# Kernel optimization log

Measured on AMD Instinct MI355X. Metric: run time of the kernel, lower is better.

## Reference

```python
import jax, jax.numpy as jnp
import numpy as np

HK, WK = 7, 11  # local_k


def _local_mask(H, W):
    # Equivalent to the torch buffer: 0 inside the hk x wk window centered on the
    # query position (for odd hk, wk), -inf outside. Shape (N, N), N = H*W.
    n = jnp.arange(H * W)
    hq, wq = n // W, n % W
    dh = jnp.abs(hq[:, None] - hq[None, :])
    dw = jnp.abs(wq[:, None] - wq[None, :])
    allowed = (dh <= HK // 2) & (dw <= WK // 2)
    return jnp.where(allowed, 0.0, -jnp.inf).astype(jnp.float32)


def setup_inputs() -> dict:
    key = jax.random.key(0)
    k1, k2, k3 = jax.random.split(key, 3)
    B, H, W, C = 8, 32, 64, 512
    N = H * W
    x = jax.random.normal(k1, (B, N, C), dtype=jnp.float32)
    qkv_w = jax.random.normal(k2, (3 * C, C), dtype=jnp.float32) * (C ** -0.5)
    proj_w = jax.random.normal(k3, (C, C), dtype=jnp.float32) * (C ** -0.5)
    proj_b = jnp.zeros((C,), dtype=jnp.float32)
    return {"x": x, "qkv_w": qkv_w, "proj_w": proj_w, "proj_b": proj_b, "H": H, "W": W}


def reference(x, qkv_w, proj_w, proj_b, H, W):
    B, N, C = x.shape
    num_heads = 8
    head_dim = C // num_heads
    scale = head_dim ** -0.5

    # qkv: Linear(dim, 3*dim, bias=False) -> (B, N, 3, heads, head_dim)
    qkv = (x @ qkv_w.T).reshape(B, N, 3, num_heads, head_dim)
    q = qkv[:, :, 0].transpose(0, 2, 1, 3) * scale  # (B, h, N, d)
    k = qkv[:, :, 1].transpose(0, 2, 1, 3)
    v = qkv[:, :, 2].transpose(0, 2, 1, 3)

    attn = jnp.einsum('bhnd,bhmd->bhnm', q, k)  # (B, h, N, N)
    attn = attn + _local_mask(H, W)  # broadcast over (B, h)
    attn = jax.nn.softmax(attn, axis=-1)

    out = jnp.einsum('bhnm,bhmd->bhnd', attn, v)  # (B, h, N, d)
    out = out.transpose(0, 2, 1, 3).reshape(B, N, C)
    return out @ proj_w.T + proj_b
```

## Files before the change

kernel.cpp:

```cpp
#include <hip/hip_runtime.h>
#include <hip/hip_bf16.h>

#define B_SZ 8
#define H_SZ 32
#define W_SZ 64
#define N_SZ 2048
#define C_SZ 512
#define NH 8
#define HD 64

using u16 = unsigned short;
typedef __attribute__((ext_vector_type(8))) short s16x8;
typedef __attribute__((ext_vector_type(4))) float f32x4;

__device__ __forceinline__ float bf2f(u16 u) {
    union { unsigned int i; float f; } c; c.i = ((unsigned int)u) << 16; return c.f;
}
__device__ __forceinline__ u16 f2bf(float f) {
    union { float f; unsigned int i; } c; c.f = f;
    unsigned int r = c.i + 0x7fffu + ((c.i >> 16) & 1u);
    return (u16)(r >> 16);
}

#define GLL16(gp, lp) __builtin_amdgcn_global_load_lds( \
    (const __attribute__((address_space(1))) unsigned int*)(gp), \
    (__attribute__((address_space(3))) unsigned int*)(lp), 16, 0, 0)

__device__ __forceinline__ int lds_off(int row, int chunk) {
    return (row * 8 + (chunk ^ (row & 7))) * 8;
}

__global__ __launch_bounds__(256) void conv_f2b(const float* __restrict__ in,
                                                u16* __restrict__ out, int n4) {
    int i = blockIdx.x * 256 + threadIdx.x;
    if (i < n4) {
        float4 v = ((const float4*)in)[i];
        ushort4 o = { f2bf(v.x), f2bf(v.y), f2bf(v.z), f2bf(v.w) };
        ((ushort4*)out)[i] = o;
    }
}
__global__ __launch_bounds__(256) void conv_qkvw(const float* __restrict__ in,
                                                 u16* __restrict__ out) {
    int i = blockIdx.x * 256 + threadIdx.x;
    float4 v = ((const float4*)in)[i];
    const float sc = (i < (512 * 512 / 4)) ? 0.125f : 1.0f;
    ushort4 o = { f2bf(v.x * sc), f2bf(v.y * sc), f2bf(v.z * sc), f2bf(v.w * sc) };
    ((ushort4*)out)[i] = o;
}

template<int MODE, int NT>
__global__ __launch_bounds__(256)
void gemm_mfma(const u16* __restrict__ A, const u16* __restrict__ Bw,
               const float* __restrict__ bias,
               u16* __restrict__ q_ws, u16* __restrict__ k_ws, u16* __restrict__ v_ws,
               float* __restrict__ outp, int K)
{
    constexpr int NJ = (NT == 128) ? 4 : 2;
    __shared__ u16 As[128 * 64];
    __shared__ u16 Bs[NT * 64];
    const int t    = threadIdx.x;
    const int m0   = blockIdx.x * 128;
    const int n0   = blockIdx.y * NT;
    const int wave = t >> 6, lane = t & 63;
    const int wm   = (wave >> 1) << 6;
    const int wn   = (wave & 1) * (NJ * 16);
    const int l16  = lane & 15, quad = lane >> 4;
    const int srow = t >> 3;
    const int sch  = (t & 7) ^ (srow & 7);

    f32x4 acc[4][NJ] = {};

    for (int k0 = 0; k0 < K; k0 += 64) {
        __syncthreads();
        #pragma unroll
        for (int g = 0; g < 4; ++g)
            GLL16(A + (size_t)(m0 + 32 * g + srow) * K + k0 + sch * 8,
                  &As[g * 2048 + t * 8]);
        #pragma unroll
        for (int g = 0; g < NT / 32; ++g)
            GLL16(Bw + (size_t)(n0 + 32 * g + srow) * K + k0 + sch * 8,
                  &Bs[g * 2048 + t * 8]);
        __syncthreads();

        s16x8 af[4][2], bf[NJ][2];
        #pragma unroll
        for (int i = 0; i < 4; ++i) {
            const int R = wm + 16 * i + l16;
            af[i][0] = *(const s16x8*)&As[lds_off(R, quad)];
            af[i][1] = *(const s16x8*)&As[lds_off(R, 4 + quad)];
        }
        #pragma unroll
        for (int j = 0; j < NJ; ++j) {
            const int R = wn + 16 * j + l16;
            bf[j][0] = *(const s16x8*)&Bs[lds_off(R, quad)];
            bf[j][1] = *(const s16x8*)&Bs[lds_off(R, 4 + quad)];
        }
        #pragma unroll
        for (int i = 0; i < 4; ++i)
            #pragma unroll
            for (int j = 0; j < NJ; ++j) {
                acc[i][j] = __builtin_amdgcn_mfma_f32_16x16x32_bf16(af[i][0], bf[j][0], acc[i][j], 0, 0, 0);
                acc[i][j] = __builtin_amdgcn_mfma_f32_16x16x32_bf16(af[i][1], bf[j][1], acc[i][j], 0, 0, 0);
            }
    }

    if (MODE == 0) {
        const int bb  = m0 >> 11;
        const int nnb = (m0 & 2047) + wm + (quad << 2);
        if (n0 >= 1024) {
            #pragma unroll
            for (int j = 0; j < NJ; ++j) {
                const int c  = n0 - 1024 + wn + 16 * j + l16;
                const int h  = c >> 6, dd = c & 63;
                u16* vp = v_ws + (((size_t)bb * NH + h) * HD + dd) * N_SZ + nnb;
                #pragma unroll
                for (int i = 0; i < 4; ++i) {
                    ushort4 st = { f2bf(acc[i][j][0]), f2bf(acc[i][j][1]),
                                   f2bf(acc[i][j][2]), f2bf(acc[i][j][3]) };
                    *(ushort4*)(vp + 16 * i) = st;
                }
            }
        } else {
            u16* T = (n0 < 512) ? q_ws : k_ws;
            #pragma unroll
            for (int j = 0; j < NJ; ++j) {
                const int gn = n0 + wn + 16 * j + l16;
                const int h  = (gn >> 6) & 7, dd = gn & 63;
                u16* tp = T + (((size_t)bb * NH + h) * N_SZ + nnb) * HD + dd;
                #pragma unroll
                for (int i = 0; i < 4; ++i)
                    #pragma unroll
                    for (int r = 0; r < 4; ++r)
                        tp[(size_t)(16 * i + r) * HD] = f2bf(acc[i][j][r]);
            }
        }
    } else {
        #pragma unroll
        for (int j = 0; j < NJ; ++j) {
            const int gn = n0 + wn + 16 * j + l16;
            const float bv = bias[gn];
            #pragma unroll
            for (int i = 0; i < 4; ++i)
                #pragma unroll
                for (int r = 0; r < 4; ++r)
                    outp[(size_t)(m0 + wm + 16 * i + (quad << 2) + r) * C_SZ + gn]
                        = acc[i][j][r] + bv;
        }
    }
}

__global__ __launch_bounds__(256)
void attn_mfma(const u16* __restrict__ q_ws, const u16* __restrict__ k_ws,
               const u16* __restrict__ vt_ws, u16* __restrict__ o_ws)
{
    __shared__ u16 Qs[64 * 64];
    __shared__ u16 Ks[64 * 64];
    __shared__ u16 Vt[64 * 64];
    __shared__ u16 Ps[4][16 * 40];

    const int t = threadIdx.x, wave = t >> 6, lane = t & 63;
    const int l16 = lane & 15, quad = lane >> 4;
    const int u  = blockIdx.x;
    const int hq = u & 31;
    const int bh = u >> 5;
    const size_t base = (size_t)bh * (N_SZ * HD);
    const int srow = t >> 3;
    const int sch  = (t & 7) ^ (srow & 7);

    const u16* qg = q_ws + base + (size_t)hq * (64 * HD);
    GLL16(qg + (size_t)srow        * 64 + sch * 8, &Qs[t * 8]);
    GLL16(qg + (size_t)(srow + 32) * 64 + sch * 8, &Qs[2048 + t * 8]);
    __syncthreads();

    const int Rq = 16 * wave + l16;
    s16x8 aQ0 = *(const s16x8*)&Qs[lds_off(Rq, quad)];
    s16x8 aQ1 = *(const s16x8*)&Qs[lds_off(Rq, 4 + quad)];

    const int kb = min(max(16 * wave - 8, 0), 32);

    f32x4 accO[4] = {};
    float lp[4] = {0.f, 0.f, 0.f, 0.f};

    const int h0 = (hq - 3 < 0) ? 0 : hq - 3;
    const int h1 = (hq + 3 > H_SZ - 1) ? H_SZ - 1 : hq + 3;

    for (int hh = h0; hh <= h1; ++hh) {
        __syncthreads();
        const u16* kg = k_ws + base + (size_t)hh * (64 * HD);
        GLL16(kg + (size_t)srow        * 64 + sch * 8, &Ks[t * 8]);
        GLL16(kg + (size_t)(srow + 32) * 64 + sch * 8, &Ks[2048 + t * 8]);
        const u16* vg = vt_ws + base + (size_t)hh * 64;
        GLL16(vg + (size_t)srow        * N_SZ + sch * 8, &Vt[t * 8]);
        GLL16(vg + (size_t)(srow + 32) * N_SZ + sch * 8, &Vt[2048 + t * 8]);
        __syncthreads();

        #pragma unroll
        for (int j = 0; j < 2; ++j) {
            const int Rk = kb + 16 * j + l16;
            s16x8 b0 = *(const s16x8*)&Ks[lds_off(Rk, quad)];
            s16x8 b1 = *(const s16x8*)&Ks[lds_off(Rk, 4 + quad)];
            f32x4 z = {0.f, 0.f, 0.f, 0.f};
            z = __builtin_amdgcn_mfma_f32_16x16x32_bf16(aQ0, b0, z, 0, 0, 0);
            z = __builtin_amdgcn_mfma_f32_16x16x32_bf16(aQ1, b1, z, 0, 0, 0);
            const int ww = kb + 16 * j + l16;
            #pragma unroll
            for (int r = 0; r < 4; ++r) {
                const int dw = ww - (16 * wave + quad * 4 + r);
                const float p = (dw * dw <= 25) ? __expf(z[r]) : 0.f;
                const u16 pb = f2bf(p);
                lp[r] += bf2f(pb);
                Ps[wave][(quad * 4 + r) * 40 + 16 * j + l16] = pb;
            }
        }

        s16x8 aP = *(const s16x8*)&Ps[wave][l16 * 40 + quad * 8];
        #pragma unroll
        for (int j = 0; j < 4; ++j) {
            const int Rv = 16 * j + l16;
            s16x8 vf = *(const s16x8*)&Vt[lds_off(Rv, (kb >> 3) + quad)];
            accO[j] = __builtin_amdgcn_mfma_f32_16x16x32_bf16(aP, vf, accO[j], 0, 0, 0);
        }
    }

    #pragma unroll
    for (int r = 0; r < 4; ++r) {
        lp[r] += __shfl_xor(lp[r], 1);
        lp[r] += __shfl_xor(lp[r], 2);
        lp[r] += __shfl_xor(lp[r], 4);
        lp[r] += __shfl_xor(lp[r], 8);
    }

    const int bb = bh >> 3, h = bh & 7;
    #pragma unroll
    for (int j = 0; j < 4; ++j) {
        #pragma unroll
        for (int r = 0; r < 4; ++r) {
            const int row = hq * 64 + 16 * wave + quad * 4 + r;
            o_ws[((size_t)bb * N_SZ + row) * C_SZ + h * 64 + 16 * j + l16]
                = f2bf(accO[j][r] / lp[r]);
        }
    }
}

extern "C" void kernel_launch(void* const* d_in, const int* in_sizes, int n_in,
                              void* d_out, int out_size, void* d_ws, size_t ws_size,
                              hipStream_t stream)
{
    const float* x      = (const float*)d_in[0];
    const float* qkv_w  = (const float*)d_in[1];
    const float* proj_w = (const float*)d_in[2];
    const float* proj_b = (const float*)d_in[3];
    float* outp = (float*)d_out;

    const size_t seg = (size_t)B_SZ * NH * N_SZ * HD;
    u16* q_ws = (u16*)d_ws;
    u16* k_ws = q_ws + seg;
    u16* v_ws = k_ws + seg;
    u16* o_ws = v_ws + seg;
    u16* xb   = o_ws + seg;
    u16* qwb  = xb + (size_t)16384 * 512;
    u16* pwb  = qwb + (size_t)1536 * 512;

    conv_f2b <<<8192, 256, 0, stream>>>(x, xb, 16384 * 512 / 4);
    conv_qkvw<<<768,  256, 0, stream>>>(qkv_w, qwb);
    conv_f2b <<<256,  256, 0, stream>>>(proj_w, pwb, 512 * 512 / 4);

    gemm_mfma<0, 128><<<dim3(128, 12), 256, 0, stream>>>(xb, qwb, nullptr,
                                                         q_ws, k_ws, v_ws, nullptr, C_SZ);
    attn_mfma<<<B_SZ * NH * H_SZ, 256, 0, stream>>>(q_ws, k_ws, v_ws, o_ws);
    gemm_mfma<1, 64><<<dim3(128, 8), 256, 0, stream>>>(o_ws, pwb, proj_b,
                                                       nullptr, nullptr, nullptr, outp, C_SZ);
}
```

Before: 186.3 us.

## Process two query rows per attention block and fuse conversion kernels

Each attention block now handles two adjacent query image rows, so every loaded K/V row tile is shared by both query rows. This cuts K/V global loads from 7 per row to about 4 per row. The LDS for Q is aliased onto the K/V buffers, and the block count is halved, which lowers parallelism. Separately, the three fp32-to-bf16 conversion launches are merged into one kernel to save launch overhead.

```diff
diff --git a/kernel.cpp b/kernel.cpp
--- a/kernel.cpp
+++ b/kernel.cpp
@@ -30,22 +30,23 @@
     return (row * 8 + (chunk ^ (row & 7))) * 8;
 }
 
-__global__ __launch_bounds__(256) void conv_f2b(const float* __restrict__ in,
-                                                u16* __restrict__ out, int n4) {
-    int i = blockIdx.x * 256 + threadIdx.x;
-    if (i < n4) {
-        float4 v = ((const float4*)in)[i];
-        ushort4 o = { f2bf(v.x), f2bf(v.y), f2bf(v.z), f2bf(v.w) };
-        ((ushort4*)out)[i] = o;
-    }
-}
-__global__ __launch_bounds__(256) void conv_qkvw(const float* __restrict__ in,
-                                                 u16* __restrict__ out) {
-    int i = blockIdx.x * 256 + threadIdx.x;
-    float4 v = ((const float4*)in)[i];
-    const float sc = (i < (512 * 512 / 4)) ? 0.125f : 1.0f;
+#define NX4 2097152
+#define NQ4 196608
+#define NP4 65536
+__global__ __launch_bounds__(256)
+void conv_all(const float* __restrict__ x, const float* __restrict__ qw,
+              const float* __restrict__ pw, u16* __restrict__ xb,
+              u16* __restrict__ qwb, u16* __restrict__ pwb)
+{
+    const int i = blockIdx.x * 256 + threadIdx.x;
+    const float* src; u16* dst; int idx; float sc = 1.0f;
+    if (i < NX4)             { src = x;  dst = xb;  idx = i; }
+    else if (i < NX4 + NQ4)  { src = qw; dst = qwb; idx = i - NX4;
+                               if (idx < 65536) sc = 0.125f; }
+    else                     { src = pw; dst = pwb; idx = i - NX4 - NQ4; }
+    const float4 v = ((const float4*)src)[idx];
     ushort4 o = { f2bf(v.x * sc), f2bf(v.y * sc), f2bf(v.z * sc), f2bf(v.w * sc) };
-    ((ushort4*)out)[i] = o;
+    ((ushort4*)dst)[idx] = o;
 }
 
 template<int MODE, int NT>
@@ -153,93 +154,114 @@
 void attn_mfma(const u16* __restrict__ q_ws, const u16* __restrict__ k_ws,
                const u16* __restrict__ vt_ws, u16* __restrict__ o_ws)
 {
-    __shared__ u16 Qs[64 * 64];
-    __shared__ u16 Ks[64 * 64];
-    __shared__ u16 Vt[64 * 64];
+    __shared__ u16 KV[2][64 * 64];
     __shared__ u16 Ps[4][16 * 40];
 
     const int t = threadIdx.x, wave = t >> 6, lane = t & 63;
     const int l16 = lane & 15, quad = lane >> 4;
     const int u  = blockIdx.x;
-    const int hq = u & 31;
-    const int bh = u >> 5;
+    const int p  = u & 15;
+    const int bh = u >> 4;
+    const int r0 = 2 * p, r1 = 2 * p + 1;
     const size_t base = (size_t)bh * (N_SZ * HD);
     const int srow = t >> 3;
     const int sch  = (t & 7) ^ (srow & 7);
 
-    const u16* qg = q_ws + base + (size_t)hq * (64 * HD);
-    GLL16(qg + (size_t)srow        * 64 + sch * 8, &Qs[t * 8]);
-    GLL16(qg + (size_t)(srow + 32) * 64 + sch * 8, &Qs[2048 + t * 8]);
+    const u16* qg = q_ws + base + (size_t)r0 * (64 * HD);
+    u16* Qst = &KV[0][0];
+    #pragma unroll
+    for (int g = 0; g < 4; ++g)
+        GLL16(qg + (size_t)(srow + 32 * g) * 64 + sch * 8, Qst + g * 2048 + t * 8);
     __syncthreads();
 
-    const int Rq = 16 * wave + l16;
-    s16x8 aQ0 = *(const s16x8*)&Qs[lds_off(Rq, quad)];
-    s16x8 aQ1 = *(const s16x8*)&Qs[lds_off(Rq, 4 + quad)];
+    s16x8 aQ[2][2];
+    #pragma unroll
+    for (int s = 0; s < 2; ++s) {
+        const int Rq = 64 * s + 16 * wave + l16;
+        aQ[s][0] = *(const s16x8*)&Qst[lds_off(Rq, quad)];
+        aQ[s][1] = *(const s16x8*)&Qst[lds_off(Rq, 4 + quad)];
+    }
 
     const int kb = min(max(16 * wave - 8, 0), 32);
 
-    f32x4 accO[4] = {};
-    float lp[4] = {0.f, 0.f, 0.f, 0.f};
-
-    const int h0 = (hq - 3 < 0) ? 0 : hq - 3;
-    const int h1 = (hq + 3 > H_SZ - 1) ? H_SZ - 1 : hq + 3;
-
-    for (int hh = h0; hh <= h1; ++hh) {
+    f32x4 accO[2][4] = {};
+    float lp[2][4] = {};
+
+    const int hlo = (r0 - 3 < 0) ? 0 : r0 - 3;
+    const int hhi = (r1 + 3 > H_SZ - 1) ? H_SZ - 1 : r1 + 3;
+
+    for (int hh = hlo; hh <= hhi; ++hh) {
         __syncthreads();
         const u16* kg = k_ws + base + (size_t)hh * (64 * HD);
-        GLL16(kg + (size_t)srow        * 64 + sch * 8, &Ks[t * 8]);
-        GLL16(kg + (size_t)(srow + 32) * 64 + sch * 8, &Ks[2048 + t * 8]);
+        GLL16(kg + (size_t)srow        * 64 + sch * 8, &KV[0][t * 8]);
+        GLL16(kg + (size_t)(srow + 32) * 64 + sch * 8, &KV[0][2048 + t * 8]);
         const u16* vg = vt_ws + base + (size_t)hh * 64;
-        GLL16(vg + (size_t)srow        * N_SZ + sch * 8, &Vt[t * 8]);
-        GLL16(vg + (size_t)(srow + 32) * N_SZ + sch * 8, &Vt[2048 + t * 8]);
-        __syncthreads();
-
+        GLL16(vg + (size_t)srow        * N_SZ + sch * 8, &KV[1][t * 8]);
+        GLL16(vg + (size_t)(srow + 32) * N_SZ + sch * 8, &KV[1][2048 + t * 8]);
+        __syncthreads();
+
+        s16x8 bK[2][2];
         #pragma unroll
         for (int j = 0; j < 2; ++j) {
             const int Rk = kb + 16 * j + l16;
-            s16x8 b0 = *(const s16x8*)&Ks[lds_off(Rk, quad)];
-            s16x8 b1 = *(const s16x8*)&Ks[lds_off(Rk, 4 + quad)];
-            f32x4 z = {0.f, 0.f, 0.f, 0.f};
-            z = __builtin_amdgcn_mfma_f32_16x16x32_bf16(aQ0, b0, z, 0, 0, 0);
-            z = __builtin_amdgcn_mfma_f32_16x16x32_bf16(aQ1, b1, z, 0, 0, 0);
-            const int ww = kb + 16 * j + l16;
+            bK[j][0] = *(const s16x8*)&KV[0][lds_off(Rk, quad)];
+            bK[j][1] = *(const s16x8*)&KV[0][lds_off(Rk, 4 + quad)];
+        }
+        s16x8 vf[4];
+        #pragma unroll
+        for (int j = 0; j < 4; ++j)
+            vf[j] = *(const s16x8*)&KV[1][lds_off(16 * j + l16, (kb >> 3) + quad)];
+
+        #pragma unroll
+        for (int s = 0; s < 2; ++s) {
+            const int dh = hh - (r0 + s);
+            if (dh * dh > 9) continue;
+            f32x4 z[2] = {{0.f,0.f,0.f,0.f},{0.f,0.f,0.f,0.f}};
+            #pragma unroll
+            for (int j = 0; j < 2; ++j) {
+                z[j] = __builtin_amdgcn_mfma_f32_16x16x32_bf16(aQ[s][0], bK[j][0], z[j], 0, 0, 0);
+                z[j] = __builtin_amdgcn_mfma_f32_16x16x32_bf16(aQ[s][1], bK[j][1], z[j], 0, 0, 0);
+            }
+            #pragma unroll
+            for (int j = 0; j < 2; ++j) {
+                const int ww = kb + 16 * j + l16;
+                #pragma unroll
+                for (int r = 0; r < 4; ++r) {
+                    const int dw = ww - (16 * wave + quad * 4 + r);
+                    const float pv = (dw * dw <= 25) ? __expf(z[j][r]) : 0.f;
+                    const u16 pb = f2bf(pv);
+                    lp[s][r] += bf2f(pb);
+                    Ps[wave][(quad * 4 + r) * 40 + 16 * j + l16] = pb;
+                }
+            }
+            s16x8 aP = *(const s16x8*)&Ps[wave][l16 * 40 + quad * 8];
+            #pragma unroll
+            for (int j = 0; j < 4; ++j)
+                accO[s][j] = __builtin_amdgcn_mfma_f32_16x16x32_bf16(aP, vf[j], accO[s][j], 0, 0, 0);
+        }
+    }
+
+    #pragma unroll
+    for (int s = 0; s < 2; ++s)
+        #pragma unroll
+        for (int r = 0; r < 4; ++r) {
+            lp[s][r] += __shfl_xor(lp[s][r], 1);
+            lp[s][r] += __shfl_xor(lp[s][r], 2);
+            lp[s][r] += __shfl_xor(lp[s][r], 4);
+            lp[s][r] += __shfl_xor(lp[s][r], 8);
+        }
+
+    const int bb = bh >> 3, h = bh & 7;
+    #pragma unroll
+    for (int s = 0; s < 2; ++s)
+        #pragma unroll
+        for (int j = 0; j < 4; ++j)
             #pragma unroll
             for (int r = 0; r < 4; ++r) {
-                const int dw = ww - (16 * wave + quad * 4 + r);
-                const float p = (dw * dw <= 25) ? __expf(z[r]) : 0.f;
-                const u16 pb = f2bf(p);
-                lp[r] += bf2f(pb);
-                Ps[wave][(quad * 4 + r) * 40 + 16 * j + l16] = pb;
-            }
-        }
-
-        s16x8 aP = *(const s16x8*)&Ps[wave][l16 * 40 + quad * 8];
-        #pragma unroll
-        for (int j = 0; j < 4; ++j) {
-            const int Rv = 16 * j + l16;
-            s16x8 vf = *(const s16x8*)&Vt[lds_off(Rv, (kb >> 3) + quad)];
-            accO[j] = __builtin_amdgcn_mfma_f32_16x16x32_bf16(aP, vf, accO[j], 0, 0, 0);
-        }
-    }
-
-    #pragma unroll
-    for (int r = 0; r < 4; ++r) {
-        lp[r] += __shfl_xor(lp[r], 1);
-        lp[r] += __shfl_xor(lp[r], 2);
-        lp[r] += __shfl_xor(lp[r], 4);
-        lp[r] += __shfl_xor(lp[r], 8);
-    }
-
-    const int bb = bh >> 3, h = bh & 7;
-    #pragma unroll
-    for (int j = 0; j < 4; ++j) {
-        #pragma unroll
-        for (int r = 0; r < 4; ++r) {
-            const int row = hq * 64 + 16 * wave + quad * 4 + r;
-            o_ws[((size_t)bb * N_SZ + row) * C_SZ + h * 64 + 16 * j + l16]
-                = f2bf(accO[j][r] / lp[r]);
-        }
-    }
+                const int row = (r0 + s) * 64 + 16 * wave + quad * 4 + r;
+                o_ws[((size_t)bb * N_SZ + row) * C_SZ + h * 64 + 16 * j + l16]
+                    = f2bf(accO[s][j][r] / lp[s][r]);
+            }
 }
 
 extern "C" void kernel_launch(void* const* d_in, const int* in_sizes, int n_in,
@@ -261,13 +283,11 @@
     u16* qwb  = xb + (size_t)16384 * 512;
     u16* pwb  = qwb + (size_t)1536 * 512;
 
-    conv_f2b <<<8192, 256, 0, stream>>>(x, xb, 16384 * 512 / 4);
-    conv_qkvw<<<768,  256, 0, stream>>>(qkv_w, qwb);
-    conv_f2b <<<256,  256, 0, stream>>>(proj_w, pwb, 512 * 512 / 4);
+    conv_all<<<9216, 256, 0, stream>>>(x, qkv_w, proj_w, xb, qwb, pwb);
 
     gemm_mfma<0, 128><<<dim3(128, 12), 256, 0, stream>>>(xb, qwb, nullptr,
                                                          q_ws, k_ws, v_ws, nullptr, C_SZ);
-    attn_mfma<<<B_SZ * NH * H_SZ, 256, 0, stream>>>(q_ws, k_ws, v_ws, o_ws);
+    attn_mfma<<<B_SZ * NH * (H_SZ / 2), 256, 0, stream>>>(q_ws, k_ws, v_ws, o_ws);
     gemm_mfma<1, 64><<<dim3(128, 8), 256, 0, stream>>>(o_ws, pwb, proj_b,
                                                        nullptr, nullptr, nullptr, outp, C_SZ);
 }
```

New measurement: 176.0 us. 5.5% less time.
